# Performance work log

Measured on AMD Instinct MI355X. Metric: run time of the kernel, lower is better.

Reference implementation:

```python
import jax, jax.numpy as jnp
import numpy as np

EMBED_DIM = 1024
ATTN_DIM = 1024


def setup_inputs() -> dict:
    key = jax.random.key(0)
    k1, k2, k3, k4 = jax.random.split(key, 4)
    scale = 1.0 / np.sqrt(EMBED_DIM)
    return {
        "embedded": jax.random.normal(k1, (4, 2048, EMBED_DIM), dtype=jnp.float32),
        # weights stored as [in, out] (torch Linear applies x @ W.T)
        "Wk": jax.random.uniform(k2, (EMBED_DIM, ATTN_DIM), dtype=jnp.float32, minval=-scale, maxval=scale),
        "Wq": jax.random.uniform(k3, (EMBED_DIM, ATTN_DIM), dtype=jnp.float32, minval=-scale, maxval=scale),
        "Wv": jax.random.uniform(k4, (EMBED_DIM, ATTN_DIM), dtype=jnp.float32, minval=-scale, maxval=scale),
    }


def reference(embedded, Wk, Wq, Wv):
    b, t, _ = embedded.shape
    k = embedded @ Wk  # [b, t, d]
    q = embedded @ Wq
    v = embedded @ Wv
    scores = jnp.einsum("btd,bsd->bts", q, k) / jnp.sqrt(jnp.float32(k.shape[-1]))
    causal = jnp.tril(jnp.ones((t, t), dtype=bool))  # [t, t]
    scores = jnp.where(causal, scores, -jnp.inf)
    w = jax.nn.softmax(scores, axis=-1)
    o = jnp.einsum("bts,bsd->btd", w, v)
    return jnp.round(o * 10000.0) / 10000.0
```

## Files before the change

### kernel.cpp

```cpp
#include <hip/hip_runtime.h>
#include <cmath>

typedef _Float16 half8 __attribute__((ext_vector_type(8)));
typedef _Float16 half4 __attribute__((ext_vector_type(4)));
typedef float floatx4 __attribute__((ext_vector_type(4)));

__device__ __forceinline__ void load_lds16(const void* g, void* l) {
  __builtin_amdgcn_global_load_lds((const __attribute__((address_space(1))) void*)g,
                                   (__attribute__((address_space(3))) void*)l, 16, 0, 0);
}


__global__ void prep_kernel(const float* __restrict__ emb, const float* __restrict__ Wq,
                            const float* __restrict__ Wk, const float* __restrict__ Wv,
                            _Float16* __restrict__ Xp, _Float16* __restrict__ Wqp,
                            _Float16* __restrict__ Wkp, _Float16* __restrict__ Wvtp) {
  int p = blockIdx.x;
  if (p < 640) {
    __shared__ _Float16 lds[16 * 1032];
    const float* src;
    _Float16* dst;
    if (p < 512)      { src = emb + (size_t)p * 16384;        dst = Xp  + (size_t)p * 16384; }
    else if (p < 576) { src = Wq + (size_t)(p - 512) * 16384; dst = Wqp + (size_t)(p - 512) * 16384; }
    else              { src = Wk + (size_t)(p - 576) * 16384; dst = Wkp + (size_t)(p - 576) * 16384; }
    for (int it = 0; it < 16; ++it) {
      int idx = it * 256 + threadIdx.x;
      int row = idx >> 8, c4 = idx & 255;
      float4 v = ((const float4*)src)[row * 256 + c4];
      half4 h;
      h[0] = (_Float16)v.x; h[1] = (_Float16)v.y; h[2] = (_Float16)v.z; h[3] = (_Float16)v.w;
      *(half4*)(lds + row * 1032 + c4 * 4) = h;
    }
    __syncthreads();
    for (int it = 0; it < 8; ++it) {
      int c = it * 256 + threadIdx.x;
      int kb = c >> 6, k16 = (c >> 4) & 3, r = c & 15;
      half8 h = *(const half8*)(lds + r * 1032 + kb * 32 + k16 * 8);
      *(half8*)(dst + (size_t)c * 8) = h;
    }
  } else {
    __shared__ float tile[32][33];
    int q = p - 640;
    int n0 = (q & 31) * 32, k0 = (q >> 5) * 32;
    int c = threadIdx.x & 31, r8 = threadIdx.x >> 5;
    for (int pp = 0; pp < 4; ++pp) {
      int r = pp * 8 + r8;
      tile[r][c] = Wv[(size_t)(k0 + r) * 1024 + n0 + c];
    }
    __syncthreads();
    if (threadIdx.x < 128) {
      int rr = threadIdx.x & 31;
      int k16 = (threadIdx.x >> 5) & 3;
      half8 h;
      for (int kk = 0; kk < 8; ++kk) h[kk] = (_Float16)tile[k16 * 8 + kk][rr];
      int n_row = n0 + rr;
      size_t chunk = ((size_t)(n_row >> 4) * 32 + (k0 >> 5)) * 64 + (k16 << 4) + (n_row & 15);
      *(half8*)(Wvtp + chunk * 8) = h;
    }
  }
}

__device__ __forceinline__ void gemm_core(const _Float16* __restrict__ Ap, int kbA, int tA0,
                                          const _Float16* __restrict__ Bp, int kbB, int tB0,
                                          int kPeriods, _Float16* sA, _Float16* sB,
                                          floatx4 acc[4][4]) {
  int tid = threadIdx.x;
  int lane = tid & 63, wave = tid >> 6;
  int wm = (wave >> 1) << 6, wn = (wave & 1) << 6;
  const _Float16* gA0 = Ap + ((size_t)(tA0 + 2 * wave) * kbA) * 512 + lane * 8;
  const _Float16* gA1 = Ap + ((size_t)(tA0 + 2 * wave + 1) * kbA) * 512 + lane * 8;
  const _Float16* gB0 = Bp + ((size_t)(tB0 + 2 * wave) * kbB) * 512 + lane * 8;
  const _Float16* gB1 = Bp + ((size_t)(tB0 + 2 * wave + 1) * kbB) * 512 + lane * 8;
  _Float16* lA = sA + wave * 2048;
  _Float16* lB = sB + wave * 2048;
  int ta = wm >> 4, tb = wn >> 4, lo = lane * 8;

  for (int kt = 0; kt < kPeriods; ++kt) {
    size_t kb = (size_t)kt * 1024;
    __syncthreads();
    load_lds16(gA0 + kb, lA);
    load_lds16(gA0 + kb + 512, lA + 512);
    load_lds16(gA1 + kb, lA + 1024);
    load_lds16(gA1 + kb + 512, lA + 1536);
    load_lds16(gB0 + kb, lB);
    load_lds16(gB0 + kb + 512, lB + 512);
    load_lds16(gB1 + kb, lB + 1024);
    load_lds16(gB1 + kb + 512, lB + 1536);
    __syncthreads();
    for (int u = 0; u < 2; ++u) {
      half8 af[4], bf[4];
      for (int i = 0; i < 4; ++i) af[i] = *(const half8*)(sA + (((ta + i) << 1) + u) * 512 + lo);
      for (int j = 0; j < 4; ++j) bf[j] = *(const half8*)(sB + (((tb + j) << 1) + u) * 512 + lo);
      for (int i = 0; i < 4; ++i)
        for (int j = 0; j < 4; ++j)
          acc[i][j] = __builtin_amdgcn_mfma_f32_16x16x32_f16(af[i], bf[j], acc[i][j], 0, 0, 0);
    }
  }
}

__global__ void mt_kernel(const _Float16* __restrict__ Wkp, const _Float16* __restrict__ Wqp,
                          _Float16* __restrict__ Mtp) {
  __shared__ __align__(16) _Float16 sA[8192];
  __shared__ __align__(16) _Float16 sB[8192];
  floatx4 acc[4][4];
  for (int i = 0; i < 4; ++i)
    for (int j = 0; j < 4; ++j) acc[i][j] = (floatx4){0.f, 0.f, 0.f, 0.f};
  int m0 = blockIdx.y * 128, n0 = blockIdx.x * 128;
  gemm_core(Wkp, 32, m0 >> 4, Wqp, 32, n0 >> 4, 16, sA, sB, acc);
  int lane = threadIdx.x & 63, wave = threadIdx.x >> 6;
  int wm = (wave >> 1) << 6, wn = (wave & 1) << 6;
  int quad = lane >> 4, cl = lane & 15;
  for (int i = 0; i < 4; ++i)
    for (int j = 0; j < 4; ++j)
      for (int rr = 0; rr < 4; ++rr) {
        int row = m0 + wm + i * 16 + quad * 4 + rr;
        int col = n0 + wn + j * 16 + cl;
        size_t chunk = ((size_t)(row >> 4) * 32 + (col >> 5)) * 64 + (((col >> 3) & 3) << 4) + (row & 15);
        Mtp[chunk * 8 + (col & 7)] = (_Float16)acc[i][j][rr];
      }
}

__global__ void proj_kernel(const _Float16* __restrict__ Xp, const _Float16* __restrict__ Bp,
                            _Float16* __restrict__ XMp, _Float16* __restrict__ Vtp) {
  __shared__ __align__(16) _Float16 sA[8192];
  __shared__ __align__(16) _Float16 sB[8192];
  floatx4 acc[4][4];
  for (int i = 0; i < 4; ++i)
    for (int j = 0; j < 4; ++j) acc[i][j] = (floatx4){0.f, 0.f, 0.f, 0.f};
  int m0 = blockIdx.y * 128, n0 = blockIdx.x * 128;
  gemm_core(Xp, 32, m0 >> 4, Bp, 32, n0 >> 4, 16, sA, sB, acc);
  int lane = threadIdx.x & 63, wave = threadIdx.x >> 6;
  int wm = (wave >> 1) << 6, wn = (wave & 1) << 6;
  int quad = lane >> 4, cl = lane & 15;
  int which = n0 >> 10;
  int colbase = (n0 & 1023) + wn;
  for (int i = 0; i < 4; ++i)
    for (int j = 0; j < 4; ++j)
      for (int rr = 0; rr < 4; ++rr) {
        int row_g = m0 + wm + i * 16 + quad * 4 + rr;
        int col = colbase + j * 16 + cl;
        _Float16 val = (_Float16)acc[i][j][rr];
        int b = row_g >> 11, t = row_g & 2047;
        if (which == 1) {
          size_t chunk = ((size_t)(col >> 4) * 64 + (t >> 5)) * 64 + (((t >> 3) & 3) << 4) + (col & 15);
          Vtp[(size_t)b * 2097152 + chunk * 8 + (t & 7)] = val;
        } else {
          size_t chunk = ((size_t)(t >> 4) * 32 + (col >> 5)) * 64 + (((col >> 3) & 3) << 4) + (t & 15);
          XMp[(size_t)b * 2097152 + chunk * 8 + (col & 7)] = val;
        }
      }
}

__global__ void qk_kernel(const _Float16* __restrict__ XMp, const _Float16* __restrict__ Xp,
                          _Float16* __restrict__ S) {
  __shared__ __align__(16) _Float16 sA[8192];
  __shared__ __align__(16) _Float16 sB[8192];
  int p = blockIdx.x, b = blockIdx.y;
  int ti = 0;
  while ((ti + 1) * (ti + 2) / 2 <= p) ++ti;
  int tj = p - ti * (ti + 1) / 2;
  const _Float16* Ab = XMp + (size_t)b * 2097152;
  const _Float16* Bb = Xp + (size_t)b * 2097152;
  _Float16* Sb = S + (size_t)b * 4194304;
  floatx4 acc[4][4];
  for (int i = 0; i < 4; ++i)
    for (int j = 0; j < 4; ++j) acc[i][j] = (floatx4){0.f, 0.f, 0.f, 0.f};
  gemm_core(Ab, 32, ti * 8, Bb, 32, tj * 8, 16, sA, sB, acc);
  int lane = threadIdx.x & 63, wave = threadIdx.x >> 6;
  int wm = (wave >> 1) << 6, wn = (wave & 1) << 6;
  int quad = lane >> 4, cl = lane & 15;
  for (int i = 0; i < 4; ++i)
    for (int j = 0; j < 4; ++j)
      for (int rr = 0; rr < 4; ++rr) {
        int row = ti * 128 + wm + i * 16 + quad * 4 + rr;
        int col = tj * 128 + wn + j * 16 + cl;
        float val = acc[i][j][rr] * 0.03125f;
        if (col > row) val = -INFINITY;
        size_t chunk = ((size_t)(row >> 4) * 64 + (col >> 5)) * 64 + (((col >> 3) & 3) << 4) + (row & 15);
        Sb[chunk * 8 + (col & 7)] = (_Float16)val;
      }
}

__global__ void softmax_kernel(_Float16* __restrict__ S) {
  __shared__ float redm[4][16];
  __shared__ float reds[4][16];
  int p = blockIdx.x, b = blockIdx.y;
  _Float16* panel = S + (size_t)b * 4194304 + (size_t)p * 32768;
  int nkb = ((p >> 3) + 1) * 4;
  int tid = threadIdx.x, lane = tid & 63, w = tid >> 6;
  int row = lane & 15;

  half8 v[16];
  float mx = -INFINITY;
  for (int it = 0; it < 16; ++it) {
    int kb = w + it * 4;
    if (kb < nkb) {
      v[it] = *(const half8*)(panel + (size_t)kb * 512 + lane * 8);
      for (int e = 0; e < 8; ++e) mx = fmaxf(mx, (float)v[it][e]);
    }
  }
  mx = fmaxf(mx, __shfl_xor(mx, 16, 64));
  mx = fmaxf(mx, __shfl_xor(mx, 32, 64));
  if (lane < 16) redm[w][lane] = mx;
  __syncthreads();
  mx = fmaxf(fmaxf(redm[0][row], redm[1][row]), fmaxf(redm[2][row], redm[3][row]));

  float sum = 0.f;
  for (int it = 0; it < 16; ++it) {
    int kb = w + it * 4;
    if (kb < nkb) {
      for (int e = 0; e < 8; ++e) {
        float ev = __expf((float)v[it][e] - mx);
        v[it][e] = (_Float16)ev;
        sum += ev;
      }
    }
  }
  sum += __shfl_xor(sum, 16, 64);
  sum += __shfl_xor(sum, 32, 64);
  if (lane < 16) reds[w][lane] = sum;
  __syncthreads();
  sum = reds[0][row] + reds[1][row] + reds[2][row] + reds[3][row];
  float inv = 1.0f / sum;

  for (int it = 0; it < 16; ++it) {
    int kb = w + it * 4;
    if (kb < nkb) {
      half8 h;
      for (int e = 0; e < 8; ++e) h[e] = (_Float16)((float)v[it][e] * inv);
      *(half8*)(panel + (size_t)kb * 512 + lane * 8) = h;
    }
  }
}

__global__ void pv_kernel(const _Float16* __restrict__ P, const _Float16* __restrict__ Vtp,
                          float* __restrict__ out) {
  __shared__ __align__(16) _Float16 sA[8192];
  __shared__ __align__(16) _Float16 sB[8192];
  int n0 = blockIdx.x * 128, b = blockIdx.z;
  int y = blockIdx.y;
  int ti = (y & 1) ? (15 - (y >> 1)) : (y >> 1);
  const _Float16* Pb = P + (size_t)b * 4194304;
  const _Float16* Vb = Vtp + (size_t)b * 2097152;
  floatx4 acc[4][4];
  for (int i = 0; i < 4; ++i)
    for (int j = 0; j < 4; ++j) acc[i][j] = (floatx4){0.f, 0.f, 0.f, 0.f};
  gemm_core(Pb, 64, ti * 8, Vb, 64, n0 >> 4, (ti + 1) * 2, sA, sB, acc);
  int lane = threadIdx.x & 63, wave = threadIdx.x >> 6;
  int wm = (wave >> 1) << 6, wn = (wave & 1) << 6;
  int quad = lane >> 4, cl = lane & 15;
  for (int i = 0; i < 4; ++i)
    for (int j = 0; j < 4; ++j)
      for (int rr = 0; rr < 4; ++rr) {
        int row = ti * 128 + wm + i * 16 + quad * 4 + rr;
        int col = n0 + wn + j * 16 + cl;
        float v = acc[i][j][rr];
        out[((size_t)b * 2048 + row) * 1024 + col] = rintf(v * 10000.f) * 1e-4f;
      }
}

extern "C" void kernel_launch(void* const* d_in, const int* in_sizes, int n_in,
                              void* d_out, int out_size, void* d_ws, size_t ws_size,
                              hipStream_t stream) {
  const float* emb = (const float*)d_in[0];
  const float* Wk = (const float*)d_in[1];
  const float* Wq = (const float*)d_in[2];
  const float* Wv = (const float*)d_in[3];
  float* out = (float*)d_out;

  _Float16* ws = (_Float16*)d_ws;
  _Float16* Xp   = ws;
  _Float16* Wqp  = Xp + (size_t)8192 * 1024;
  _Float16* Wkp  = Wqp + (size_t)1024 * 1024;
  _Float16* Mtp  = Wkp + (size_t)1024 * 1024;
  _Float16* Wvtp = Mtp + (size_t)1024 * 1024;
  _Float16* XMp  = Wvtp + (size_t)1024 * 1024;
  _Float16* Vtp  = XMp + (size_t)8192 * 1024;
  _Float16* S    = Vtp + (size_t)8192 * 1024;

  prep_kernel<<<1664, 256, 0, stream>>>(emb, Wq, Wk, Wv, Xp, Wqp, Wkp, Wvtp);
  mt_kernel<<<dim3(8, 8), 256, 0, stream>>>(Wkp, Wqp, Mtp);
  proj_kernel<<<dim3(16, 64), 256, 0, stream>>>(Xp, Mtp, XMp, Vtp);
  qk_kernel<<<dim3(136, 4), 256, 0, stream>>>(XMp, Xp, S);
  softmax_kernel<<<dim3(128, 4), 256, 0, stream>>>(S);
  pv_kernel<<<dim3(8, 16, 4), 256, 0, stream>>>(S, Vtp, out);
}
```

Baseline: 250.3 us.

## Halve K-step per sync, swizzle QK tile order, use 256-row PV tiles with 8 waves

The shared GEMM core now stages one 32-wide K chunk per barrier pair instead of two, halving LDS footprint per block so more blocks can be resident. QK block indices are permuted to interleave triangle tiles across the grid. PV switches to 512-thread blocks computing 256x128 output tiles, so each V tile is reused across twice as many rows. This needs softmax to zero-pad the upper triangle up to 256-column boundaries. The exchange is more barriers per unit of K work and fewer, larger PV blocks with coarser causal granularity, which means some extra zero multiplies.

```diff
diff --git a/kernel.cpp b/kernel.cpp
--- a/kernel.cpp
+++ b/kernel.cpp
@@ -62,7 +62,7 @@
 
 __device__ __forceinline__ void gemm_core(const _Float16* __restrict__ Ap, int kbA, int tA0,
                                           const _Float16* __restrict__ Bp, int kbB, int tB0,
-                                          int kPeriods, _Float16* sA, _Float16* sB,
+                                          int kIters, _Float16* sA, _Float16* sB,
                                           floatx4 acc[4][4]) {
   int tid = threadIdx.x;
   int lane = tid & 63, wave = tid >> 6;
@@ -71,42 +71,69 @@
   const _Float16* gA1 = Ap + ((size_t)(tA0 + 2 * wave + 1) * kbA) * 512 + lane * 8;
   const _Float16* gB0 = Bp + ((size_t)(tB0 + 2 * wave) * kbB) * 512 + lane * 8;
   const _Float16* gB1 = Bp + ((size_t)(tB0 + 2 * wave + 1) * kbB) * 512 + lane * 8;
-  _Float16* lA = sA + wave * 2048;
-  _Float16* lB = sB + wave * 2048;
+  _Float16* lA0 = sA + wave * 1024;
+  _Float16* lA1 = lA0 + 512;
+  _Float16* lB0 = sB + wave * 1024;
+  _Float16* lB1 = lB0 + 512;
   int ta = wm >> 4, tb = wn >> 4, lo = lane * 8;
 
-  for (int kt = 0; kt < kPeriods; ++kt) {
-    size_t kb = (size_t)kt * 1024;
-    __syncthreads();
-    load_lds16(gA0 + kb, lA);
-    load_lds16(gA0 + kb + 512, lA + 512);
-    load_lds16(gA1 + kb, lA + 1024);
-    load_lds16(gA1 + kb + 512, lA + 1536);
-    load_lds16(gB0 + kb, lB);
-    load_lds16(gB0 + kb + 512, lB + 512);
-    load_lds16(gB1 + kb, lB + 1024);
-    load_lds16(gB1 + kb + 512, lB + 1536);
-    __syncthreads();
-    for (int u = 0; u < 2; ++u) {
-      half8 af[4], bf[4];
-      for (int i = 0; i < 4; ++i) af[i] = *(const half8*)(sA + (((ta + i) << 1) + u) * 512 + lo);
-      for (int j = 0; j < 4; ++j) bf[j] = *(const half8*)(sB + (((tb + j) << 1) + u) * 512 + lo);
-      for (int i = 0; i < 4; ++i)
-        for (int j = 0; j < 4; ++j)
-          acc[i][j] = __builtin_amdgcn_mfma_f32_16x16x32_f16(af[i], bf[j], acc[i][j], 0, 0, 0);
-    }
+  for (int kt = 0; kt < kIters; ++kt) {
+    size_t kb = (size_t)kt * 512;
+    __syncthreads();
+    load_lds16(gA0 + kb, lA0);
+    load_lds16(gA1 + kb, lA1);
+    load_lds16(gB0 + kb, lB0);
+    load_lds16(gB1 + kb, lB1);
+    __syncthreads();
+    half8 af[4], bf[4];
+    for (int i = 0; i < 4; ++i) af[i] = *(const half8*)(sA + (ta + i) * 512 + lo);
+    for (int j = 0; j < 4; ++j) bf[j] = *(const half8*)(sB + (tb + j) * 512 + lo);
+    for (int i = 0; i < 4; ++i)
+      for (int j = 0; j < 4; ++j)
+        acc[i][j] = __builtin_amdgcn_mfma_f32_16x16x32_f16(af[i], bf[j], acc[i][j], 0, 0, 0);
+  }
+}
+
+__device__ __forceinline__ void gemm_core_w(const _Float16* __restrict__ Ap, int kbA, int tA0,
+                                            const _Float16* __restrict__ Bp, int kbB, int tB0,
+                                            int kIters, _Float16* sA, _Float16* sB,
+                                            floatx4 acc[4][4]) {
+  int tid = threadIdx.x;
+  int lane = tid & 63, wave = tid >> 6;
+  int wm = (wave >> 1) << 6, wn = (wave & 1) << 6;
+  const _Float16* gA0 = Ap + ((size_t)(tA0 + 2 * wave) * kbA) * 512 + lane * 8;
+  const _Float16* gA1 = Ap + ((size_t)(tA0 + 2 * wave + 1) * kbA) * 512 + lane * 8;
+  const _Float16* gB0 = Bp + ((size_t)(tB0 + wave) * kbB) * 512 + lane * 8;
+  _Float16* lA0 = sA + wave * 1024;
+  _Float16* lA1 = lA0 + 512;
+  _Float16* lB0 = sB + wave * 512;
+  int ta = wm >> 4, tb = wn >> 4, lo = lane * 8;
+
+  for (int kt = 0; kt < kIters; ++kt) {
+    size_t kb = (size_t)kt * 512;
+    __syncthreads();
+    load_lds16(gA0 + kb, lA0);
+    load_lds16(gA1 + kb, lA1);
+    load_lds16(gB0 + kb, lB0);
+    __syncthreads();
+    half8 af[4], bf[4];
+    for (int i = 0; i < 4; ++i) af[i] = *(const half8*)(sA + (ta + i) * 512 + lo);
+    for (int j = 0; j < 4; ++j) bf[j] = *(const half8*)(sB + (tb + j) * 512 + lo);
+    for (int i = 0; i < 4; ++i)
+      for (int j = 0; j < 4; ++j)
+        acc[i][j] = __builtin_amdgcn_mfma_f32_16x16x32_f16(af[i], bf[j], acc[i][j], 0, 0, 0);
   }
 }
 
 __global__ void mt_kernel(const _Float16* __restrict__ Wkp, const _Float16* __restrict__ Wqp,
                           _Float16* __restrict__ Mtp) {
-  __shared__ __align__(16) _Float16 sA[8192];
-  __shared__ __align__(16) _Float16 sB[8192];
+  __shared__ __align__(16) _Float16 sA[4096];
+  __shared__ __align__(16) _Float16 sB[4096];
   floatx4 acc[4][4];
   for (int i = 0; i < 4; ++i)
     for (int j = 0; j < 4; ++j) acc[i][j] = (floatx4){0.f, 0.f, 0.f, 0.f};
   int m0 = blockIdx.y * 128, n0 = blockIdx.x * 128;
-  gemm_core(Wkp, 32, m0 >> 4, Wqp, 32, n0 >> 4, 16, sA, sB, acc);
+  gemm_core(Wkp, 32, m0 >> 4, Wqp, 32, n0 >> 4, 32, sA, sB, acc);
   int lane = threadIdx.x & 63, wave = threadIdx.x >> 6;
   int wm = (wave >> 1) << 6, wn = (wave & 1) << 6;
   int quad = lane >> 4, cl = lane & 15;
@@ -122,13 +149,13 @@
 
 __global__ void proj_kernel(const _Float16* __restrict__ Xp, const _Float16* __restrict__ Bp,
                             _Float16* __restrict__ XMp, _Float16* __restrict__ Vtp) {
-  __shared__ __align__(16) _Float16 sA[8192];
-  __shared__ __align__(16) _Float16 sB[8192];
+  __shared__ __align__(16) _Float16 sA[4096];
+  __shared__ __align__(16) _Float16 sB[4096];
   floatx4 acc[4][4];
   for (int i = 0; i < 4; ++i)
     for (int j = 0; j < 4; ++j) acc[i][j] = (floatx4){0.f, 0.f, 0.f, 0.f};
   int m0 = blockIdx.y * 128, n0 = blockIdx.x * 128;
-  gemm_core(Xp, 32, m0 >> 4, Bp, 32, n0 >> 4, 16, sA, sB, acc);
+  gemm_core(Xp, 32, m0 >> 4, Bp, 32, n0 >> 4, 32, sA, sB, acc);
   int lane = threadIdx.x & 63, wave = threadIdx.x >> 6;
   int wm = (wave >> 1) << 6, wn = (wave & 1) << 6;
   int quad = lane >> 4, cl = lane & 15;
@@ -153,9 +180,10 @@
 
 __global__ void qk_kernel(const _Float16* __restrict__ XMp, const _Float16* __restrict__ Xp,
                           _Float16* __restrict__ S) {
-  __shared__ __align__(16) _Float16 sA[8192];
-  __shared__ __align__(16) _Float16 sB[8192];
-  int p = blockIdx.x, b = blockIdx.y;
+  __shared__ __align__(16) _Float16 sA[4096];
+  __shared__ __align__(16) _Float16 sB[4096];
+  int x = blockIdx.x, b = blockIdx.y;
+  int p = (x & 7) * 17 + (x >> 3);
   int ti = 0;
   while ((ti + 1) * (ti + 2) / 2 <= p) ++ti;
   int tj = p - ti * (ti + 1) / 2;
@@ -165,7 +193,7 @@
   floatx4 acc[4][4];
   for (int i = 0; i < 4; ++i)
     for (int j = 0; j < 4; ++j) acc[i][j] = (floatx4){0.f, 0.f, 0.f, 0.f};
-  gemm_core(Ab, 32, ti * 8, Bb, 32, tj * 8, 16, sA, sB, acc);
+  gemm_core(Ab, 32, ti * 8, Bb, 32, tj * 8, 32, sA, sB, acc);
   int lane = threadIdx.x & 63, wave = threadIdx.x >> 6;
   int wm = (wave >> 1) << 6, wn = (wave & 1) << 6;
   int quad = lane >> 4, cl = lane & 15;
@@ -187,6 +215,7 @@
   int p = blockIdx.x, b = blockIdx.y;
   _Float16* panel = S + (size_t)b * 4194304 + (size_t)p * 32768;
   int nkb = ((p >> 3) + 1) * 4;
+  int nkbPad = ((p >> 4) + 1) * 8;
   int tid = threadIdx.x, lane = tid & 63, w = tid >> 6;
   int row = lane & 15;
 
@@ -229,6 +258,10 @@
       half8 h;
       for (int e = 0; e < 8; ++e) h[e] = (_Float16)((float)v[it][e] * inv);
       *(half8*)(panel + (size_t)kb * 512 + lane * 8) = h;
+    } else if (kb < nkbPad) {
+      half8 z;
+      for (int e = 0; e < 8; ++e) z[e] = (_Float16)0.f;
+      *(half8*)(panel + (size_t)kb * 512 + lane * 8) = z;
     }
   }
 }
@@ -236,23 +269,23 @@
 __global__ void pv_kernel(const _Float16* __restrict__ P, const _Float16* __restrict__ Vtp,
                           float* __restrict__ out) {
   __shared__ __align__(16) _Float16 sA[8192];
-  __shared__ __align__(16) _Float16 sB[8192];
+  __shared__ __align__(16) _Float16 sB[4096];
   int n0 = blockIdx.x * 128, b = blockIdx.z;
   int y = blockIdx.y;
-  int ti = (y & 1) ? (15 - (y >> 1)) : (y >> 1);
+  int TI = (y & 1) ? (7 - (y >> 1)) : (y >> 1);
   const _Float16* Pb = P + (size_t)b * 4194304;
   const _Float16* Vb = Vtp + (size_t)b * 2097152;
   floatx4 acc[4][4];
   for (int i = 0; i < 4; ++i)
     for (int j = 0; j < 4; ++j) acc[i][j] = (floatx4){0.f, 0.f, 0.f, 0.f};
-  gemm_core(Pb, 64, ti * 8, Vb, 64, n0 >> 4, (ti + 1) * 2, sA, sB, acc);
+  gemm_core_w(Pb, 64, TI * 16, Vb, 64, n0 >> 4, (TI + 1) * 8, sA, sB, acc);
   int lane = threadIdx.x & 63, wave = threadIdx.x >> 6;
   int wm = (wave >> 1) << 6, wn = (wave & 1) << 6;
   int quad = lane >> 4, cl = lane & 15;
   for (int i = 0; i < 4; ++i)
     for (int j = 0; j < 4; ++j)
       for (int rr = 0; rr < 4; ++rr) {
-        int row = ti * 128 + wm + i * 16 + quad * 4 + rr;
+        int row = TI * 256 + wm + i * 16 + quad * 4 + rr;
         int col = n0 + wn + j * 16 + cl;
         float v = acc[i][j][rr];
         out[((size_t)b * 2048 + row) * 1024 + col] = rintf(v * 10000.f) * 1e-4f;
@@ -283,5 +316,5 @@
   proj_kernel<<<dim3(16, 64), 256, 0, stream>>>(Xp, Mtp, XMp, Vtp);
   qk_kernel<<<dim3(136, 4), 256, 0, stream>>>(XMp, Xp, S);
   softmax_kernel<<<dim3(128, 4), 256, 0, stream>>>(S);
-  pv_kernel<<<dim3(8, 16, 4), 256, 0, stream>>>(S, Vtp, out);
-}
+  pv_kernel<<<dim3(8, 8, 4), 512, 0, stream>>>(S, Vtp, out);
+}
```

Result: slower. 262.2 us (+4.7%).
